# Optimization experiments

Hardware: AMD Instinct MI355X
Metric: run time of the kernel (lower is better)

## Reference

```python
import jax, jax.numpy as jnp
import numpy as np


def setup_inputs() -> dict:
    key = jax.random.key(0)
    ks = jax.random.split(key, 8)
    B, Q, K, F, FV, C = 8, 2048, 2048, 512, 512, 2
    q = jax.random.normal(ks[0], (B, Q, F), dtype=jnp.float32)
    k = jax.random.normal(ks[1], (B, K, F), dtype=jnp.float32)
    v = jax.random.normal(ks[2], (B, K, FV), dtype=jnp.float32)
    coords_q = jax.random.uniform(ks[3], (B, Q, C), dtype=jnp.float32)
    coords_k = jax.random.uniform(ks[4], (B, K, C), dtype=jnp.float32)
    attn_mask = jax.random.randint(ks[5], (B, Q, K), 0, 2).astype(bool)
    alibi_mask = jax.random.randint(ks[6], (B, Q, K), 0, 2).astype(bool)
    bias_scale = jax.random.uniform(ks[7], (1,), dtype=jnp.float32)
    return {"q": q, "k": k, "v": v, "coords_q": coords_q, "coords_k": coords_k,
            "attn_mask": attn_mask, "alibi_mask": alibi_mask, "bias_scale": bias_scale}


def reference(q, k, v, coords_q, coords_k, attn_mask, alibi_mask, bias_scale):
    # scaled dot-product logits: [B, Q, K]
    scale = k.shape[-1] ** -0.5
    weight_logits = jnp.einsum('bqf,bkf->bqk', q, k) * scale
    # pairwise Euclidean coordinate distances: [B, Q, K]
    diff = coords_q[:, :, None, :] - coords_k[:, None, :, :]
    distances = jnp.linalg.norm(diff, axis=-1)
    # _RunningMeanScaler in eval mode divides by running_mean == 1 (identity)
    scaled_distances = distances * bias_scale  # bias_scale broadcasts from [1]
    scaled_distances = jnp.where(alibi_mask, 0.0, scaled_distances)
    weights = jax.nn.softmax(weight_logits, axis=-1)
    # post-softmax bias subtraction + masking (non-standard attention)
    weights = jnp.where(attn_mask, 0.0, weights - scaled_distances)
    attention = jnp.einsum('bqk,bkf->bqf', weights, v)
    return attention
```

## Files before the change

### kernel.cpp

```cpp
#include <hip/hip_runtime.h>
#include <hip/hip_bf16.h>
#include <math.h>

#define BN  8
#define QN  2048
#define KN  2048
#define FN  512
#define FVN 512

typedef __bf16 bf16x8 __attribute__((ext_vector_type(8)));
typedef __bf16 bf16x4v __attribute__((ext_vector_type(4)));
typedef float  f32x4  __attribute__((ext_vector_type(4)));

__device__ inline bf16x8 pack8(float4 a, float4 b) {
  bf16x8 r;
  r[0] = (__bf16)a.x; r[1] = (__bf16)a.y; r[2] = (__bf16)a.z; r[3] = (__bf16)a.w;
  r[4] = (__bf16)b.x; r[5] = (__bf16)b.y; r[6] = (__bf16)b.z; r[7] = (__bf16)b.w;
  return r;
}

__device__ __forceinline__ void g2l16(const __bf16* g, __bf16* l) {
  __builtin_amdgcn_global_load_lds(
      (const __attribute__((address_space(1))) void*)g,
      (__attribute__((address_space(3))) void*)l,
      16, 0, 0);
}

__global__ __launch_bounds__(256) void prep(
    const float* __restrict__ qm, const float* __restrict__ km,
    const float* __restrict__ vm,
    __bf16* __restrict__ qb, __bf16* __restrict__ kb, __bf16* __restrict__ Vt) {
  const int tid = threadIdx.x;
  if (blockIdx.y == 0) {
    const size_t idx = ((size_t)blockIdx.x * 256 + tid) * 8;
    const float scale = 0.044194173824159216f;
    float4 a = *(const float4*)(qm + idx);
    float4 b = *(const float4*)(qm + idx + 4);
    a.x *= scale; a.y *= scale; a.z *= scale; a.w *= scale;
    b.x *= scale; b.y *= scale; b.z *= scale; b.w *= scale;
    *(bf16x8*)(qb + idx) = pack8(a, b);
  } else if (blockIdx.y == 1) {
    const size_t idx = ((size_t)blockIdx.x * 256 + tid) * 8;
    float4 a = *(const float4*)(km + idx);
    float4 b = *(const float4*)(km + idx + 4);
    *(bf16x8*)(kb + idx) = pack8(a, b);
  } else {
    const int bx = blockIdx.x;
    if (bx >= (KN / 64) * (FVN / 64) * BN) return;
    const int b  = bx >> 8;
    const int f0 = ((bx >> 5) & 7) * 64;
    const int k0 = (bx & 31) * 64;
    __shared__ float tile[64][65];
    const int r = tid >> 4;
    const int c = (tid & 15) * 4;
#pragma unroll
    for (int i = 0; i < 4; i++) {
      float4 u = *(const float4*)(vm + ((size_t)b * KN + k0 + r + i * 16) * FVN + f0 + c);
      tile[r + i * 16][c] = u.x; tile[r + i * 16][c + 1] = u.y;
      tile[r + i * 16][c + 2] = u.z; tile[r + i * 16][c + 3] = u.w;
    }
    __syncthreads();
#pragma unroll
    for (int i = 0; i < 4; i++) {
      int fv = r + i * 16;
      bf16x4v w;
      w[0] = (__bf16)tile[c][fv];     w[1] = (__bf16)tile[c + 1][fv];
      w[2] = (__bf16)tile[c + 2][fv]; w[3] = (__bf16)tile[c + 3][fv];
      *(bf16x4v*)(Vt + ((size_t)b * FVN + f0 + fv) * KN + k0 + c) = w;
    }
  }
}

__global__ __launch_bounds__(256) void gemm_s(
    const __bf16* __restrict__ qb, const __bf16* __restrict__ kb,
    __bf16* __restrict__ Sws, int b0, int q0, int qchunk) {
  __shared__ __align__(16) __bf16 As[2][128][32];
  __shared__ __align__(16) __bf16 Bs[2][128][32];
  const int tid = threadIdx.x;
  const int lane = tid & 63, wave = tid >> 6;
  const int wq = (wave & 1) * 64, wk = (wave >> 1) * 64;
  const int qt = blockIdx.x * 128, kt = blockIdx.y * 128;
  const int z = blockIdx.z, b = b0 + z;
  __bf16* S = Sws + (size_t)z * qchunk * KN;
  const __bf16* Ab = qb + ((size_t)b * QN + q0 + qt) * FN;
  const __bf16* Bb = kb + ((size_t)b * KN + kt) * FN;
  const int srow = lane >> 2;
  const int scol = (lane & 3) * 8;
  const int r = lane & 15, quad = lane >> 4;
  f32x4 acc[4][4] = {};
  for (int f0 = 0; f0 < FN; f0 += 64) {
    __syncthreads();
#pragma unroll
    for (int h = 0; h < 2; h++) {
      const int co = f0 + h * 32 + scol;
      g2l16(Ab + (size_t)(wave * 32 + srow) * FN + co,      &As[h][wave * 32][0]);
      g2l16(Ab + (size_t)(wave * 32 + 16 + srow) * FN + co, &As[h][wave * 32 + 16][0]);
      g2l16(Bb + (size_t)(wave * 32 + srow) * FN + co,      &Bs[h][wave * 32][0]);
      g2l16(Bb + (size_t)(wave * 32 + 16 + srow) * FN + co, &Bs[h][wave * 32 + 16][0]);
    }
    __syncthreads();
#pragma unroll
    for (int h = 0; h < 2; h++) {
      bf16x8 af[4], bf[4];
#pragma unroll
      for (int i = 0; i < 4; i++) af[i] = *(bf16x8*)&As[h][wq + i * 16 + r][quad * 8];
#pragma unroll
      for (int j = 0; j < 4; j++) bf[j] = *(bf16x8*)&Bs[h][wk + j * 16 + r][quad * 8];
#pragma unroll
      for (int i = 0; i < 4; i++)
#pragma unroll
        for (int j = 0; j < 4; j++)
          acc[i][j] = __builtin_amdgcn_mfma_f32_16x16x32_bf16(af[i], bf[j], acc[i][j], 0, 0, 0);
    }
  }
#pragma unroll
  for (int i = 0; i < 4; i++)
#pragma unroll
    for (int j = 0; j < 4; j++)
#pragma unroll
      for (int t = 0; t < 4; t++) {
        int qq = qt + wq + i * 16 + quad * 4 + t;
        int kk = kt + wk + j * 16 + r;
        S[(size_t)qq * KN + kk] = (__bf16)acc[i][j][t];
      }
}

__global__ __launch_bounds__(256) void softmax_w(
    __bf16* __restrict__ Sws,
    const float* __restrict__ cq, const float* __restrict__ ck,
    const int* __restrict__ attn, const int* __restrict__ alibi,
    const float* __restrict__ bsp, int b0, int q0, int qchunk) {
  const int z = blockIdx.z, b = b0 + z;
  const int lane = threadIdx.x & 63, wave = threadIdx.x >> 6;
  const int ql = blockIdx.x * 4 + wave;
  const int qg = q0 + ql;
  __bf16* Srow = Sws + ((size_t)z * qchunk + ql) * KN;
  const int* arow = attn + ((size_t)b * QN + qg) * KN;
  const int* lrow = alibi + ((size_t)b * QN + qg) * KN;
  const float* ckb = ck + (size_t)b * KN * 2;
  bf16x8 s8[4];
#pragma unroll
  for (int c = 0; c < 4; c++) s8[c] = *(bf16x8*)(Srow + c * 512 + lane * 8);
  float p[32];
  float sum = 0.f;
#pragma unroll
  for (int c = 0; c < 4; c++)
#pragma unroll
    for (int i = 0; i < 8; i++) { p[c * 8 + i] = __expf((float)s8[c][i]); sum += p[c * 8 + i]; }
  for (int o = 32; o > 0; o >>= 1) sum += __shfl_xor(sum, o);
  const float inv = 1.0f / sum;
  const float qx = cq[((size_t)b * QN + qg) * 2 + 0];
  const float qy = cq[((size_t)b * QN + qg) * 2 + 1];
  const float bs = bsp[0];
#pragma unroll
  for (int c = 0; c < 4; c++) {
    const int k0 = c * 512 + lane * 8;
    int4 am0 = *(const int4*)(arow + k0);
    int4 am1 = *(const int4*)(arow + k0 + 4);
    int4 al0 = *(const int4*)(lrow + k0);
    int4 al1 = *(const int4*)(lrow + k0 + 4);
    float4 c0 = *(const float4*)(ckb + (size_t)k0 * 2);
    float4 c1 = *(const float4*)(ckb + (size_t)k0 * 2 + 4);
    float4 c2 = *(const float4*)(ckb + (size_t)k0 * 2 + 8);
    float4 c3 = *(const float4*)(ckb + (size_t)k0 * 2 + 12);
    int   am[8] = {am0.x, am0.y, am0.z, am0.w, am1.x, am1.y, am1.z, am1.w};
    int   al[8] = {al0.x, al0.y, al0.z, al0.w, al1.x, al1.y, al1.z, al1.w};
    float kx[8] = {c0.x, c0.z, c1.x, c1.z, c2.x, c2.z, c3.x, c3.z};
    float ky[8] = {c0.y, c0.w, c1.y, c1.w, c2.y, c2.w, c3.y, c3.w};
    bf16x8 w8;
#pragma unroll
    for (int j = 0; j < 8; j++) {
      float dx = qx - kx[j], dy = qy - ky[j];
      float sd = al[j] ? 0.f : sqrtf(dx * dx + dy * dy) * bs;
      float w = am[j] ? 0.f : (p[c * 8 + j] * inv - sd);
      w8[j] = (__bf16)w;
    }
    *(bf16x8*)(Srow + k0) = w8;
  }
}

__global__ __launch_bounds__(256) void gemm_w(
    const __bf16* __restrict__ W, const __bf16* __restrict__ Vt,
    float* __restrict__ out, int b0, int q0, int qchunk) {
  __shared__ __align__(16) __bf16 As[2][128][32];
  __shared__ __align__(16) __bf16 Bs[2][128][32];
  const int tid = threadIdx.x;
  const int lane = tid & 63, wave = tid >> 6;
  const int wq = (wave & 1) * 64, wf = (wave >> 1) * 64;
  const int qt = blockIdx.x * 128, ft = blockIdx.y * 128;
  const int z = blockIdx.z, b = b0 + z;
  const __bf16* Ab = W + ((size_t)z * qchunk + qt) * KN;
  const __bf16* Bb = Vt + ((size_t)b * FVN + ft) * KN;
  const int srow = lane >> 2;
  const int scol = (lane & 3) * 8;
  const int r = lane & 15, quad = lane >> 4;
  f32x4 acc[4][4] = {};
  for (int k0 = 0; k0 < KN; k0 += 64) {
    __syncthreads();
#pragma unroll
    for (int h = 0; h < 2; h++) {
      const int co = k0 + h * 32 + scol;
      g2l16(Ab + (size_t)(wave * 32 + srow) * KN + co,      &As[h][wave * 32][0]);
      g2l16(Ab + (size_t)(wave * 32 + 16 + srow) * KN + co, &As[h][wave * 32 + 16][0]);
      g2l16(Bb + (size_t)(wave * 32 + srow) * KN + co,      &Bs[h][wave * 32][0]);
      g2l16(Bb + (size_t)(wave * 32 + 16 + srow) * KN + co, &Bs[h][wave * 32 + 16][0]);
    }
    __syncthreads();
#pragma unroll
    for (int h = 0; h < 2; h++) {
      bf16x8 af[4], bf[4];
#pragma unroll
      for (int i = 0; i < 4; i++) af[i] = *(bf16x8*)&As[h][wq + i * 16 + r][quad * 8];
#pragma unroll
      for (int j = 0; j < 4; j++) bf[j] = *(bf16x8*)&Bs[h][wf + j * 16 + r][quad * 8];
#pragma unroll
      for (int i = 0; i < 4; i++)
#pragma unroll
        for (int j = 0; j < 4; j++)
          acc[i][j] = __builtin_amdgcn_mfma_f32_16x16x32_bf16(af[i], bf[j], acc[i][j], 0, 0, 0);
    }
  }
#pragma unroll
  for (int i = 0; i < 4; i++)
#pragma unroll
    for (int j = 0; j < 4; j++)
#pragma unroll
      for (int t = 0; t < 4; t++) {
        int qq = q0 + qt + wq + i * 16 + quad * 4 + t;
        int fv = ft + wf + j * 16 + r;
        out[((size_t)b * QN + qq) * FVN + fv] = acc[i][j][t];
      }
}

extern "C" void kernel_launch(void* const* d_in, const int* in_sizes, int n_in,
                              void* d_out, int out_size, void* d_ws, size_t ws_size,
                              hipStream_t stream) {
  (void)in_sizes; (void)n_in; (void)out_size;
  const float* qm   = (const float*)d_in[0];
  const float* km   = (const float*)d_in[1];
  const float* vm   = (const float*)d_in[2];
  const float* cq   = (const float*)d_in[3];
  const float* ck   = (const float*)d_in[4];
  const int*   attn = (const int*)d_in[5];
  const int*   alibi= (const int*)d_in[6];
  const float* bsp  = (const float*)d_in[7];
  float* out = (float*)d_out;

  __bf16* qb  = (__bf16*)d_ws;
  __bf16* kb  = qb + (size_t)BN * QN * FN;
  __bf16* Vt  = kb + (size_t)BN * KN * FN;
  __bf16* Sws = Vt + (size_t)BN * FVN * KN;
  const size_t fixed = ((size_t)BN * QN * FN + (size_t)BN * KN * FN +
                        (size_t)BN * FVN * KN) * 2;
  int nb = BN, qc = QN;
  while (nb > 1 && fixed + (size_t)nb * qc * KN * 2 > ws_size) nb >>= 1;
  while (qc > 128 && fixed + (size_t)nb * qc * KN * 2 > ws_size) qc >>= 1;

  prep<<<dim3((BN * QN * FN) / 2048, 3), 256, 0, stream>>>(qm, km, vm, qb, kb, Vt);
  for (int b0 = 0; b0 < BN; b0 += nb) {
    for (int q0 = 0; q0 < QN; q0 += qc) {
      gemm_s<<<dim3(qc / 128, KN / 128, nb), 256, 0, stream>>>(qb, kb, Sws, b0, q0, qc);
      softmax_w<<<dim3(qc / 4, 1, nb), 256, 0, stream>>>(Sws, cq, ck, attn, alibi, bsp, b0, q0, qc);
      gemm_w<<<dim3(qc / 128, FVN / 128, nb), 256, 0, stream>>>(Sws, Vt, out, b0, q0, qc);
    }
  }
}
```

Before: 468.0 us.

## Fuse softmax normalization and bias masking into the PV GEMM with atomic row sums

Softmax denominators are now computed in the QK GEMM epilogue through warp shuffles and atomicAdd into a zeroed sums buffer. The separate softmax kernel is removed, and the new gemm_wv kernel computes exp, distance bias and masking on the fly while staging the A tile. Each block covers 64 query rows and all 512 value columns, so the S matrix is read once and never written back as weights. The cost is float atomics, one extra prep branch to zero the sums, a larger LDS footprint and 512-thread blocks with fewer blocks in flight.

```diff
diff --git a/kernel.cpp b/kernel.cpp
--- a/kernel.cpp
+++ b/kernel.cpp
@@ -29,7 +29,8 @@
 __global__ __launch_bounds__(256) void prep(
     const float* __restrict__ qm, const float* __restrict__ km,
     const float* __restrict__ vm,
-    __bf16* __restrict__ qb, __bf16* __restrict__ kb, __bf16* __restrict__ Vt) {
+    __bf16* __restrict__ qb, __bf16* __restrict__ kb, __bf16* __restrict__ Vt,
+    float* __restrict__ sums) {
   const int tid = threadIdx.x;
   if (blockIdx.y == 0) {
     const size_t idx = ((size_t)blockIdx.x * 256 + tid) * 8;
@@ -44,7 +45,7 @@
     float4 a = *(const float4*)(km + idx);
     float4 b = *(const float4*)(km + idx + 4);
     *(bf16x8*)(kb + idx) = pack8(a, b);
-  } else {
+  } else if (blockIdx.y == 2) {
     const int bx = blockIdx.x;
     if (bx >= (KN / 64) * (FVN / 64) * BN) return;
     const int b  = bx >> 8;
@@ -68,12 +69,18 @@
       w[2] = (__bf16)tile[c + 2][fv]; w[3] = (__bf16)tile[c + 3][fv];
       *(bf16x4v*)(Vt + ((size_t)b * FVN + f0 + fv) * KN + k0 + c) = w;
     }
+  } else {
+    if (blockIdx.x < (BN * QN) / 1024) {
+      float4 z4; z4.x = 0.f; z4.y = 0.f; z4.z = 0.f; z4.w = 0.f;
+      ((float4*)sums)[(size_t)blockIdx.x * 256 + tid] = z4;
+    }
   }
 }
 
 __global__ __launch_bounds__(256) void gemm_s(
     const __bf16* __restrict__ qb, const __bf16* __restrict__ kb,
-    __bf16* __restrict__ Sws, int b0, int q0, int qchunk) {
+    __bf16* __restrict__ Sws, float* __restrict__ sums,
+    int b0, int q0, int qchunk) {
   __shared__ __align__(16) __bf16 As[2][128][32];
   __shared__ __align__(16) __bf16 Bs[2][128][32];
   const int tid = threadIdx.x;
@@ -123,112 +130,126 @@
         int kk = kt + wk + j * 16 + r;
         S[(size_t)qq * KN + kk] = (__bf16)acc[i][j][t];
       }
-}
-
-__global__ __launch_bounds__(256) void softmax_w(
-    __bf16* __restrict__ Sws,
+#pragma unroll
+  for (int i = 0; i < 4; i++)
+#pragma unroll
+    for (int t = 0; t < 4; t++) {
+      float part = 0.f;
+#pragma unroll
+      for (int j = 0; j < 4; j++) part += __expf(acc[i][j][t]);
+      part += __shfl_xor(part, 1);
+      part += __shfl_xor(part, 2);
+      part += __shfl_xor(part, 4);
+      part += __shfl_xor(part, 8);
+      if (r == 0)
+        atomicAdd(&sums[(size_t)b * QN + q0 + qt + wq + i * 16 + quad * 4 + t], part);
+    }
+}
+
+__global__ __launch_bounds__(512) void gemm_wv(
+    const __bf16* __restrict__ Sws, const __bf16* __restrict__ Vt,
+    const float* __restrict__ sums,
     const float* __restrict__ cq, const float* __restrict__ ck,
     const int* __restrict__ attn, const int* __restrict__ alibi,
-    const float* __restrict__ bsp, int b0, int q0, int qchunk) {
-  const int z = blockIdx.z, b = b0 + z;
-  const int lane = threadIdx.x & 63, wave = threadIdx.x >> 6;
-  const int ql = blockIdx.x * 4 + wave;
-  const int qg = q0 + ql;
-  __bf16* Srow = Sws + ((size_t)z * qchunk + ql) * KN;
+    const float* __restrict__ bsp, float* __restrict__ out,
+    int b0, int q0, int qchunk, int nb) {
+  __shared__ __align__(16) __bf16 As[2][64][32];
+  __shared__ __align__(16) __bf16 Bs[2][512][32];
+  const int tid = threadIdx.x;
+  const int lane = tid & 63, wave = tid >> 6;
+  const int flat = blockIdx.x;
+  const int z = flat & (nb - 1);
+  const int b = b0 + z;
+  const int qt = (flat / nb) * 64;
+  const int arow_i = tid >> 3;
+  const int ac8 = tid & 7;
+  const int qg = q0 + qt + arow_i;
+  const __bf16* Srow = Sws + ((size_t)z * qchunk + qt + arow_i) * KN;
   const int* arow = attn + ((size_t)b * QN + qg) * KN;
   const int* lrow = alibi + ((size_t)b * QN + qg) * KN;
   const float* ckb = ck + (size_t)b * KN * 2;
-  bf16x8 s8[4];
-#pragma unroll
-  for (int c = 0; c < 4; c++) s8[c] = *(bf16x8*)(Srow + c * 512 + lane * 8);
-  float p[32];
-  float sum = 0.f;
-#pragma unroll
-  for (int c = 0; c < 4; c++)
-#pragma unroll
-    for (int i = 0; i < 8; i++) { p[c * 8 + i] = __expf((float)s8[c][i]); sum += p[c * 8 + i]; }
-  for (int o = 32; o > 0; o >>= 1) sum += __shfl_xor(sum, o);
-  const float inv = 1.0f / sum;
+  const float inv = 1.0f / sums[(size_t)b * QN + qg];
   const float qx = cq[((size_t)b * QN + qg) * 2 + 0];
   const float qy = cq[((size_t)b * QN + qg) * 2 + 1];
   const float bs = bsp[0];
-#pragma unroll
-  for (int c = 0; c < 4; c++) {
-    const int k0 = c * 512 + lane * 8;
-    int4 am0 = *(const int4*)(arow + k0);
-    int4 am1 = *(const int4*)(arow + k0 + 4);
-    int4 al0 = *(const int4*)(lrow + k0);
-    int4 al1 = *(const int4*)(lrow + k0 + 4);
-    float4 c0 = *(const float4*)(ckb + (size_t)k0 * 2);
-    float4 c1 = *(const float4*)(ckb + (size_t)k0 * 2 + 4);
-    float4 c2 = *(const float4*)(ckb + (size_t)k0 * 2 + 8);
-    float4 c3 = *(const float4*)(ckb + (size_t)k0 * 2 + 12);
-    int   am[8] = {am0.x, am0.y, am0.z, am0.w, am1.x, am1.y, am1.z, am1.w};
-    int   al[8] = {al0.x, al0.y, al0.z, al0.w, al1.x, al1.y, al1.z, al1.w};
-    float kx[8] = {c0.x, c0.z, c1.x, c1.z, c2.x, c2.z, c3.x, c3.z};
-    float ky[8] = {c0.y, c0.w, c1.y, c1.w, c2.y, c2.w, c3.y, c3.w};
-    bf16x8 w8;
-#pragma unroll
-    for (int j = 0; j < 8; j++) {
-      float dx = qx - kx[j], dy = qy - ky[j];
-      float sd = al[j] ? 0.f : sqrtf(dx * dx + dy * dy) * bs;
-      float w = am[j] ? 0.f : (p[c * 8 + j] * inv - sd);
-      w8[j] = (__bf16)w;
-    }
-    *(bf16x8*)(Srow + k0) = w8;
-  }
-}
-
-__global__ __launch_bounds__(256) void gemm_w(
-    const __bf16* __restrict__ W, const __bf16* __restrict__ Vt,
-    float* __restrict__ out, int b0, int q0, int qchunk) {
-  __shared__ __align__(16) __bf16 As[2][128][32];
-  __shared__ __align__(16) __bf16 Bs[2][128][32];
-  const int tid = threadIdx.x;
-  const int lane = tid & 63, wave = tid >> 6;
-  const int wq = (wave & 1) * 64, wf = (wave >> 1) * 64;
-  const int qt = blockIdx.x * 128, ft = blockIdx.y * 128;
-  const int z = blockIdx.z, b = b0 + z;
-  const __bf16* Ab = W + ((size_t)z * qchunk + qt) * KN;
-  const __bf16* Bb = Vt + ((size_t)b * FVN + ft) * KN;
-  const int srow = lane >> 2;
-  const int scol = (lane & 3) * 8;
+  const int srow = tid >> 2;
+  const int scol = (tid & 3) * 8;
+  const __bf16* Bb = Vt + (size_t)b * FVN * KN;
   const int r = lane & 15, quad = lane >> 4;
-  f32x4 acc[4][4] = {};
-  for (int k0 = 0; k0 < KN; k0 += 64) {
-    __syncthreads();
+  const int wq2 = (wave & 1) * 32;
+  const int wf  = (wave >> 1) * 128;
+
+  f32x4 acc[2][8] = {};
+  bf16x8 s8; int4 am0, am1, al0, al1; float4 c0, c1, c2, c3;
+  {
+    const int kk = ac8 * 8;
+    s8  = *(const bf16x8*)(Srow + kk);
+    am0 = *(const int4*)(arow + kk); am1 = *(const int4*)(arow + kk + 4);
+    al0 = *(const int4*)(lrow + kk); al1 = *(const int4*)(lrow + kk + 4);
+    c0 = *(const float4*)(ckb + (size_t)kk * 2);
+    c1 = *(const float4*)(ckb + (size_t)kk * 2 + 4);
+    c2 = *(const float4*)(ckb + (size_t)kk * 2 + 8);
+    c3 = *(const float4*)(ckb + (size_t)kk * 2 + 12);
+  }
+  for (int t = 0; t < KN / 64; ++t) {
+    __syncthreads();
+    {
+      int   am[8] = {am0.x, am0.y, am0.z, am0.w, am1.x, am1.y, am1.z, am1.w};
+      int   al[8] = {al0.x, al0.y, al0.z, al0.w, al1.x, al1.y, al1.z, al1.w};
+      float kx[8] = {c0.x, c0.z, c1.x, c1.z, c2.x, c2.z, c3.x, c3.z};
+      float ky[8] = {c0.y, c0.w, c1.y, c1.w, c2.y, c2.w, c3.y, c3.w};
+      bf16x8 w8;
+#pragma unroll
+      for (int j = 0; j < 8; j++) {
+        float p = __expf((float)s8[j]);
+        float dx = qx - kx[j], dy = qy - ky[j];
+        float sd = al[j] ? 0.f : sqrtf(dx * dx + dy * dy) * bs;
+        float w = am[j] ? 0.f : (p * inv - sd);
+        w8[j] = (__bf16)w;
+      }
+      *(bf16x8*)&As[ac8 >> 2][arow_i][(ac8 & 3) * 8] = w8;
+    }
+    const int k0 = t * 64;
+#pragma unroll
+    for (int h = 0; h < 2; h++)
+#pragma unroll
+      for (int rr = 0; rr < 4; rr++)
+        g2l16(Bb + (size_t)(rr * 128 + srow) * KN + k0 + h * 32 + scol,
+              &Bs[h][rr * 128 + wave * 16][0]);
+    __syncthreads();
+    if (t + 1 < KN / 64) {
+      const int kk = (t + 1) * 64 + ac8 * 8;
+      s8  = *(const bf16x8*)(Srow + kk);
+      am0 = *(const int4*)(arow + kk); am1 = *(const int4*)(arow + kk + 4);
+      al0 = *(const int4*)(lrow + kk); al1 = *(const int4*)(lrow + kk + 4);
+      c0 = *(const float4*)(ckb + (size_t)kk * 2);
+      c1 = *(const float4*)(ckb + (size_t)kk * 2 + 4);
+      c2 = *(const float4*)(ckb + (size_t)kk * 2 + 8);
+      c3 = *(const float4*)(ckb + (size_t)kk * 2 + 12);
+    }
 #pragma unroll
     for (int h = 0; h < 2; h++) {
-      const int co = k0 + h * 32 + scol;
-      g2l16(Ab + (size_t)(wave * 32 + srow) * KN + co,      &As[h][wave * 32][0]);
-      g2l16(Ab + (size_t)(wave * 32 + 16 + srow) * KN + co, &As[h][wave * 32 + 16][0]);
-      g2l16(Bb + (size_t)(wave * 32 + srow) * KN + co,      &Bs[h][wave * 32][0]);
-      g2l16(Bb + (size_t)(wave * 32 + 16 + srow) * KN + co, &Bs[h][wave * 32 + 16][0]);
-    }
-    __syncthreads();
-#pragma unroll
-    for (int h = 0; h < 2; h++) {
-      bf16x8 af[4], bf[4];
-#pragma unroll
-      for (int i = 0; i < 4; i++) af[i] = *(bf16x8*)&As[h][wq + i * 16 + r][quad * 8];
-#pragma unroll
-      for (int j = 0; j < 4; j++) bf[j] = *(bf16x8*)&Bs[h][wf + j * 16 + r][quad * 8];
-#pragma unroll
-      for (int i = 0; i < 4; i++)
-#pragma unroll
-        for (int j = 0; j < 4; j++)
-          acc[i][j] = __builtin_amdgcn_mfma_f32_16x16x32_bf16(af[i], bf[j], acc[i][j], 0, 0, 0);
-    }
-  }
-#pragma unroll
-  for (int i = 0; i < 4; i++)
-#pragma unroll
-    for (int j = 0; j < 4; j++)
-#pragma unroll
-      for (int t = 0; t < 4; t++) {
-        int qq = q0 + qt + wq + i * 16 + quad * 4 + t;
-        int fv = ft + wf + j * 16 + r;
-        out[((size_t)b * QN + qq) * FVN + fv] = acc[i][j][t];
+      bf16x8 af[2], bv[8];
+#pragma unroll
+      for (int i = 0; i < 2; i++) af[i] = *(bf16x8*)&As[h][wq2 + i * 16 + r][quad * 8];
+#pragma unroll
+      for (int j = 0; j < 8; j++) bv[j] = *(bf16x8*)&Bs[h][wf + j * 16 + r][quad * 8];
+#pragma unroll
+      for (int i = 0; i < 2; i++)
+#pragma unroll
+        for (int j = 0; j < 8; j++)
+          acc[i][j] = __builtin_amdgcn_mfma_f32_16x16x32_bf16(af[i], bv[j], acc[i][j], 0, 0, 0);
+    }
+  }
+#pragma unroll
+  for (int i = 0; i < 2; i++)
+#pragma unroll
+    for (int j = 0; j < 8; j++)
+#pragma unroll
+      for (int t4 = 0; t4 < 4; t4++) {
+        int qq = q0 + qt + wq2 + i * 16 + quad * 4 + t4;
+        int fv = wf + j * 16 + r;
+        out[((size_t)b * QN + qq) * FVN + fv] = acc[i][j][t4];
       }
 }
 
@@ -249,19 +270,20 @@
   __bf16* qb  = (__bf16*)d_ws;
   __bf16* kb  = qb + (size_t)BN * QN * FN;
   __bf16* Vt  = kb + (size_t)BN * KN * FN;
-  __bf16* Sws = Vt + (size_t)BN * FVN * KN;
+  float*  sums = (float*)(Vt + (size_t)BN * FVN * KN);
+  __bf16* Sws = (__bf16*)(sums + (size_t)BN * QN);
   const size_t fixed = ((size_t)BN * QN * FN + (size_t)BN * KN * FN +
-                        (size_t)BN * FVN * KN) * 2;
+                        (size_t)BN * FVN * KN) * 2 + (size_t)BN * QN * 4;
   int nb = BN, qc = QN;
   while (nb > 1 && fixed + (size_t)nb * qc * KN * 2 > ws_size) nb >>= 1;
   while (qc > 128 && fixed + (size_t)nb * qc * KN * 2 > ws_size) qc >>= 1;
 
-  prep<<<dim3((BN * QN * FN) / 2048, 3), 256, 0, stream>>>(qm, km, vm, qb, kb, Vt);
+  prep<<<dim3((BN * QN * FN) / 2048, 4), 256, 0, stream>>>(qm, km, vm, qb, kb, Vt, sums);
   for (int b0 = 0; b0 < BN; b0 += nb) {
     for (int q0 = 0; q0 < QN; q0 += qc) {
-      gemm_s<<<dim3(qc / 128, KN / 128, nb), 256, 0, stream>>>(qb, kb, Sws, b0, q0, qc);
-      softmax_w<<<dim3(qc / 4, 1, nb), 256, 0, stream>>>(Sws, cq, ck, attn, alibi, bsp, b0, q0, qc);
-      gemm_w<<<dim3(qc / 128, FVN / 128, nb), 256, 0, stream>>>(Sws, Vt, out, b0, q0, qc);
-    }
-  }
-}
+      gemm_s<<<dim3(qc / 128, KN / 128, nb), 256, 0, stream>>>(qb, kb, Sws, sums, b0, q0, qc);
+      gemm_wv<<<dim3(nb * (qc / 64)), 512, 0, stream>>>(Sws, Vt, sums, cq, ck, attn,
+                                                        alibi, bsp, out, b0, q0, qc, nb);
+    }
+  }
+}
```

New measurement: 499.6 us. 6.8% more time.

## Fuse softmax row-sum into QK GEMM epilogue via atomics; stage key coords in LDS

Applied to the files above, without the earlier changes.

The QK GEMM epilogue now computes exp of each fp32 logit, reduces across lanes, and atomically adds per-row partial sums into a workspace buffer, which a new prep branch zeroes. The softmax kernel no longer does its own cross-lane sum reduction; it reads the precomputed sum and issues all mask and score loads up front. It also stages key coordinates into shared memory once per block instead of having every wave reload them from global memory. The cost is extra exp work and atomics in the GEMM, plus a row sum taken from fp32 accumulators rather than from the bf16-rounded scores used for the numerators, which slightly changes rounding.

```diff
diff --git a/kernel.cpp b/kernel.cpp
--- a/kernel.cpp
+++ b/kernel.cpp
@@ -29,7 +29,8 @@
 __global__ __launch_bounds__(256) void prep(
     const float* __restrict__ qm, const float* __restrict__ km,
     const float* __restrict__ vm,
-    __bf16* __restrict__ qb, __bf16* __restrict__ kb, __bf16* __restrict__ Vt) {
+    __bf16* __restrict__ qb, __bf16* __restrict__ kb, __bf16* __restrict__ Vt,
+    float* __restrict__ sums) {
   const int tid = threadIdx.x;
   if (blockIdx.y == 0) {
     const size_t idx = ((size_t)blockIdx.x * 256 + tid) * 8;
@@ -44,7 +45,7 @@
     float4 a = *(const float4*)(km + idx);
     float4 b = *(const float4*)(km + idx + 4);
     *(bf16x8*)(kb + idx) = pack8(a, b);
-  } else {
+  } else if (blockIdx.y == 2) {
     const int bx = blockIdx.x;
     if (bx >= (KN / 64) * (FVN / 64) * BN) return;
     const int b  = bx >> 8;
@@ -68,12 +69,18 @@
       w[2] = (__bf16)tile[c + 2][fv]; w[3] = (__bf16)tile[c + 3][fv];
       *(bf16x4v*)(Vt + ((size_t)b * FVN + f0 + fv) * KN + k0 + c) = w;
     }
+  } else {
+    if (blockIdx.x < (BN * QN) / 1024) {
+      float4 z4; z4.x = 0.f; z4.y = 0.f; z4.z = 0.f; z4.w = 0.f;
+      ((float4*)sums)[(size_t)blockIdx.x * 256 + tid] = z4;
+    }
   }
 }
 
 __global__ __launch_bounds__(256) void gemm_s(
     const __bf16* __restrict__ qb, const __bf16* __restrict__ kb,
-    __bf16* __restrict__ Sws, int b0, int q0, int qchunk) {
+    __bf16* __restrict__ Sws, float* __restrict__ sums,
+    int b0, int q0, int qchunk) {
   __shared__ __align__(16) __bf16 As[2][128][32];
   __shared__ __align__(16) __bf16 Bs[2][128][32];
   const int tid = threadIdx.x;
@@ -123,13 +130,29 @@
         int kk = kt + wk + j * 16 + r;
         S[(size_t)qq * KN + kk] = (__bf16)acc[i][j][t];
       }
+#pragma unroll
+  for (int i = 0; i < 4; i++)
+#pragma unroll
+    for (int t = 0; t < 4; t++) {
+      float part = 0.f;
+#pragma unroll
+      for (int j = 0; j < 4; j++) part += __expf(acc[i][j][t]);
+      part += __shfl_xor(part, 1);
+      part += __shfl_xor(part, 2);
+      part += __shfl_xor(part, 4);
+      part += __shfl_xor(part, 8);
+      if (r == 0)
+        atomicAdd(&sums[(size_t)b * QN + q0 + qt + wq + i * 16 + quad * 4 + t], part);
+    }
 }
 
 __global__ __launch_bounds__(256) void softmax_w(
     __bf16* __restrict__ Sws,
     const float* __restrict__ cq, const float* __restrict__ ck,
     const int* __restrict__ attn, const int* __restrict__ alibi,
-    const float* __restrict__ bsp, int b0, int q0, int qchunk) {
+    const float* __restrict__ bsp, const float* __restrict__ sums,
+    int b0, int q0, int qchunk) {
+  __shared__ float ckx[KN], cky[KN];
   const int z = blockIdx.z, b = b0 + z;
   const int lane = threadIdx.x & 63, wave = threadIdx.x >> 6;
   const int ql = blockIdx.x * 4 + wave;
@@ -138,42 +161,44 @@
   const int* arow = attn + ((size_t)b * QN + qg) * KN;
   const int* lrow = alibi + ((size_t)b * QN + qg) * KN;
   const float* ckb = ck + (size_t)b * KN * 2;
-  bf16x8 s8[4];
-#pragma unroll
-  for (int c = 0; c < 4; c++) s8[c] = *(bf16x8*)(Srow + c * 512 + lane * 8);
-  float p[32];
-  float sum = 0.f;
-#pragma unroll
-  for (int c = 0; c < 4; c++)
-#pragma unroll
-    for (int i = 0; i < 8; i++) { p[c * 8 + i] = __expf((float)s8[c][i]); sum += p[c * 8 + i]; }
-  for (int o = 32; o > 0; o >>= 1) sum += __shfl_xor(sum, o);
-  const float inv = 1.0f / sum;
+  bf16x8 s8[4]; int4 am[8], al[8];
+#pragma unroll
+  for (int c = 0; c < 4; c++) {
+    const int k0 = c * 512 + lane * 8;
+    s8[c]       = *(const bf16x8*)(Srow + k0);
+    am[c * 2]     = *(const int4*)(arow + k0);
+    am[c * 2 + 1] = *(const int4*)(arow + k0 + 4);
+    al[c * 2]     = *(const int4*)(lrow + k0);
+    al[c * 2 + 1] = *(const int4*)(lrow + k0 + 4);
+  }
+  const float inv = 1.0f / sums[(size_t)b * QN + qg];
   const float qx = cq[((size_t)b * QN + qg) * 2 + 0];
   const float qy = cq[((size_t)b * QN + qg) * 2 + 1];
   const float bs = bsp[0];
+  for (int i = threadIdx.x; i < KN / 2; i += 256) {
+    float4 u = *(const float4*)(ckb + (size_t)i * 4);
+    ckx[2 * i] = u.x;     cky[2 * i] = u.y;
+    ckx[2 * i + 1] = u.z; cky[2 * i + 1] = u.w;
+  }
+  __syncthreads();
 #pragma unroll
   for (int c = 0; c < 4; c++) {
     const int k0 = c * 512 + lane * 8;
-    int4 am0 = *(const int4*)(arow + k0);
-    int4 am1 = *(const int4*)(arow + k0 + 4);
-    int4 al0 = *(const int4*)(lrow + k0);
-    int4 al1 = *(const int4*)(lrow + k0 + 4);
-    float4 c0 = *(const float4*)(ckb + (size_t)k0 * 2);
-    float4 c1 = *(const float4*)(ckb + (size_t)k0 * 2 + 4);
-    float4 c2 = *(const float4*)(ckb + (size_t)k0 * 2 + 8);
-    float4 c3 = *(const float4*)(ckb + (size_t)k0 * 2 + 12);
-    int   am[8] = {am0.x, am0.y, am0.z, am0.w, am1.x, am1.y, am1.z, am1.w};
-    int   al[8] = {al0.x, al0.y, al0.z, al0.w, al1.x, al1.y, al1.z, al1.w};
-    float kx[8] = {c0.x, c0.z, c1.x, c1.z, c2.x, c2.z, c3.x, c3.z};
-    float ky[8] = {c0.y, c0.w, c1.y, c1.w, c2.y, c2.w, c3.y, c3.w};
+    float4 x0 = *(const float4*)&ckx[k0]; float4 x1 = *(const float4*)&ckx[k0 + 4];
+    float4 y0 = *(const float4*)&cky[k0]; float4 y1 = *(const float4*)&cky[k0 + 4];
+    float kx[8] = {x0.x, x0.y, x0.z, x0.w, x1.x, x1.y, x1.z, x1.w};
+    float ky[8] = {y0.x, y0.y, y0.z, y0.w, y1.x, y1.y, y1.z, y1.w};
+    int amv[8] = {am[c * 2].x, am[c * 2].y, am[c * 2].z, am[c * 2].w,
+                  am[c * 2 + 1].x, am[c * 2 + 1].y, am[c * 2 + 1].z, am[c * 2 + 1].w};
+    int alv[8] = {al[c * 2].x, al[c * 2].y, al[c * 2].z, al[c * 2].w,
+                  al[c * 2 + 1].x, al[c * 2 + 1].y, al[c * 2 + 1].z, al[c * 2 + 1].w};
     bf16x8 w8;
 #pragma unroll
     for (int j = 0; j < 8; j++) {
+      float p = __expf((float)s8[c][j]) * inv;
       float dx = qx - kx[j], dy = qy - ky[j];
-      float sd = al[j] ? 0.f : sqrtf(dx * dx + dy * dy) * bs;
-      float w = am[j] ? 0.f : (p[c * 8 + j] * inv - sd);
-      w8[j] = (__bf16)w;
+      float sd = alv[j] ? 0.f : sqrtf(dx * dx + dy * dy) * bs;
+      w8[j] = (__bf16)(amv[j] ? 0.f : (p - sd));
     }
     *(bf16x8*)(Srow + k0) = w8;
   }
@@ -249,18 +274,20 @@
   __bf16* qb  = (__bf16*)d_ws;
   __bf16* kb  = qb + (size_t)BN * QN * FN;
   __bf16* Vt  = kb + (size_t)BN * KN * FN;
-  __bf16* Sws = Vt + (size_t)BN * FVN * KN;
+  float*  sums = (float*)(Vt + (size_t)BN * FVN * KN);
+  __bf16* Sws = (__bf16*)(sums + (size_t)BN * QN);
   const size_t fixed = ((size_t)BN * QN * FN + (size_t)BN * KN * FN +
-                        (size_t)BN * FVN * KN) * 2;
+                        (size_t)BN * FVN * KN) * 2 + (size_t)BN * QN * 4;
   int nb = BN, qc = QN;
   while (nb > 1 && fixed + (size_t)nb * qc * KN * 2 > ws_size) nb >>= 1;
   while (qc > 128 && fixed + (size_t)nb * qc * KN * 2 > ws_size) qc >>= 1;
 
-  prep<<<dim3((BN * QN * FN) / 2048, 3), 256, 0, stream>>>(qm, km, vm, qb, kb, Vt);
+  prep<<<dim3((BN * QN * FN) / 2048, 4), 256, 0, stream>>>(qm, km, vm, qb, kb, Vt, sums);
   for (int b0 = 0; b0 < BN; b0 += nb) {
     for (int q0 = 0; q0 < QN; q0 += qc) {
-      gemm_s<<<dim3(qc / 128, KN / 128, nb), 256, 0, stream>>>(qb, kb, Sws, b0, q0, qc);
-      softmax_w<<<dim3(qc / 4, 1, nb), 256, 0, stream>>>(Sws, cq, ck, attn, alibi, bsp, b0, q0, qc);
+      gemm_s<<<dim3(qc / 128, KN / 128, nb), 256, 0, stream>>>(qb, kb, Sws, sums, b0, q0, qc);
+      softmax_w<<<dim3(qc / 4, 1, nb), 256, 0, stream>>>(Sws, cq, ck, attn, alibi, bsp,
+                                                         sums, b0, q0, qc);
       gemm_w<<<dim3(qc / 128, FVN / 128, nb), 256, 0, stream>>>(Sws, Vt, out, b0, q0, qc);
     }
   }
```

Measured after the change: 481.4 us. 2.9% more time.
